# Kernel tuning notes

Hardware: AMD Instinct MI355X
Metric: run time of the kernel (lower is better)

The kernel has to match this reference:

```python
import jax, jax.numpy as jnp
import numpy as np

BN_EPS = 1e-5
NORM_EPS = 1e-12  # F.normalize eps
NUM_HEADS = 8
QUERY_DIM = 256
TOP_K = 16


def _l2norm(x):
    n = jnp.linalg.norm(x, axis=-1, keepdims=True)
    return x / jnp.maximum(n, NORM_EPS)


def setup_inputs() -> dict:
    key = jax.random.key(0)
    ks = jax.random.split(key, 8)
    B, S, D, O, N = 2, 512, 1024, 1024, 16384
    return {
        "hidden_states": jax.random.normal(ks[0], (B, S, D), jnp.float32),
        "Wq": jax.random.normal(ks[1], (D, NUM_HEADS * QUERY_DIM), jnp.float32) * 0.02,
        "bq": jnp.zeros((NUM_HEADS * QUERY_DIM,), jnp.float32),
        "bn_gamma": jnp.ones((QUERY_DIM,), jnp.float32),
        "bn_beta": jnp.zeros((QUERY_DIM,), jnp.float32),
        "sub_keys0": jax.random.normal(ks[2], (128, 128), jnp.float32) * 0.02,
        "sub_keys1": jax.random.normal(ks[3], (128, 128), jnp.float32) * 0.02,
        "expert_down": jax.random.normal(ks[4], (N, D), jnp.float32) * 0.02,
        "expert_up": jax.random.normal(ks[5], (N, O), jnp.float32) * 0.02,
    }


def reference(hidden_states, Wq, bq, bn_gamma, bn_beta, sub_keys0, sub_keys1, expert_down, expert_up):
    B, S, D = hidden_states.shape
    H, QD, K = NUM_HEADS, QUERY_DIM, TOP_K

    # query projection -> [B,S,H,QD]
    q = (hidden_states @ Wq + bq).reshape(B, S, H, QD)

    # BatchNorm1d over flattened (B*S*H, QD), training-mode batch stats (biased var)
    qf = q.reshape(-1, QD)
    mean = qf.mean(axis=0)
    var = qf.var(axis=0)
    qf = (qf - mean) * jax.lax.rsqrt(var + BN_EPS) * bn_gamma + bn_beta
    q = qf.reshape(B, S, H, QD)

    # split query into two halves, L2-normalize queries and keys, sub-scores
    half = QD // 2
    s0 = jnp.einsum('bshd,nd->bshn', _l2norm(q[..., :half]), _l2norm(sub_keys0))  # [B,S,H,128]
    s1 = jnp.einsum('bshd,nd->bshn', _l2norm(q[..., half:]), _l2norm(sub_keys1))  # [B,S,H,128]

    # cartesian-product scores: flat expert idx = i*128 + j (matches meshgrid 'ij')
    total = (s0[..., :, None] + s1[..., None, :]).reshape(B, S, H, -1)  # [B,S,H,16384]

    top_scores, top_idx = jax.lax.top_k(total, K)  # [B,S,H,K]
    w = jax.nn.softmax(top_scores, axis=-1)

    dw = expert_down[top_idx]  # [B,S,H,K,D]  (expert_hidden_size = 1)
    uw = expert_up[top_idx]    # [B,S,H,K,O]

    ei = jnp.einsum('bshkd,bsd->bshk', dw, hidden_states)  # per-expert scalar hidden
    eo = jax.nn.gelu(ei, approximate=False)                # F.gelu default = erf
    out = jnp.einsum('bshko,bshk,bshk->bso', uw, eo, w)    # weighted sum over K and H
    return out
```

## Files before the change

kernel.cpp:

```cpp
#include <hip/hip_runtime.h>
#include <math.h>

typedef unsigned long long u64;
typedef unsigned int u32;
typedef unsigned short ushort_t;
typedef _Float16 half8 __attribute__((ext_vector_type(8)));
typedef float f32x4 __attribute__((ext_vector_type(4)));

#define TOKENS 1024
#define DDIM   1024
#define NHEAD  8
#define QD     256
#define HQD    2048
#define NROWS  8192
#define NKEY   128
#define TOPK   16

#define QSCALE 256.0f
#define QINVS  (1.0f / 65536.0f)

__device__ __forceinline__ ushort_t f2bf(float f) {
    u32 u = __float_as_uint(f);
    u32 r = (u + 0x7FFFu + ((u >> 16) & 1u)) >> 16;
    return (ushort_t)r;
}
__device__ __forceinline__ float bf_lo(u32 w) { return __uint_as_float(w << 16); }
__device__ __forceinline__ float bf_hi(u32 w) { return __uint_as_float(w & 0xFFFF0000u); }

__device__ __forceinline__ void hsplit(float x, ushort_t& h, ushort_t& l) {
    _Float16 hh = (_Float16)x;
    float r = x - (float)hh;
    _Float16 ll = (_Float16)r;
    union { _Float16 f; ushort_t u; } c1, c2;
    c1.f = hh; c2.f = ll;
    h = c1.u; l = c2.u;
}

__device__ __forceinline__ u32 ordf(float v) {
    u32 u = __float_as_uint(v);
    return (u & 0x80000000u) ? ~u : (u | 0x80000000u);
}
__device__ __forceinline__ u64 mkkey2(float v, u32 idx) {
    return ((u64)ordf(v) << 32) | (u64)(0xFFFFFFFFu - idx);
}

template<int NTHR, int ITERS>
__device__ __forceinline__ void cvt_chunk(int gcb, int tid,
                                          const float* __restrict__ down,
                                          const float* __restrict__ up,
                                          ushort_t* __restrict__ downb,
                                          ushort_t* __restrict__ upb) {
    const float* src = (gcb < 1024) ? down : up;
    ushort_t* dst = (gcb < 1024) ? downb : upb;
    const size_t base4 = (size_t)(gcb & 1023) * 4096;
    const float4* s4 = (const float4*)src;
    ushort4* d4 = (ushort4*)dst;
#pragma unroll 4
    for (int it = 0; it < ITERS; it++) {
        size_t i = base4 + (size_t)it * NTHR + tid;
        float4 v = s4[i];
        ushort4 o;
        o.x = f2bf(v.x); o.y = f2bf(v.y); o.z = f2bf(v.z); o.w = f2bf(v.w);
        d4[i] = o;
    }
}

__global__ __launch_bounds__(256) void k_prep1(
    const float* __restrict__ A, const float* __restrict__ W,
    ushort_t* __restrict__ Ab, ushort_t* __restrict__ Wt,
    const float* __restrict__ sk0, const float* __restrict__ sk1,
    float* __restrict__ k0n, float* __restrict__ k1n)
{
    __shared__ __align__(16) char praw[18464];
    const int bid = blockIdx.x;
    const int tid = threadIdx.x;

    if (bid < 128) {
#pragma unroll
        for (int i = 0; i < 8; i++) {
            const int row = bid * 8 + i;
            float4 v = *(const float4*)(A + (size_t)row * 1024 + tid * 4);
            ushort4 h, l;
            hsplit(v.x * QSCALE, h.x, l.x);
            hsplit(v.y * QSCALE, h.y, l.y);
            hsplit(v.z * QSCALE, h.z, l.z);
            hsplit(v.w * QSCALE, h.w, l.w);
            *(ushort4*)(Ab + (size_t)row * 2048 + tid * 4) = h;
            *(ushort4*)(Ab + (size_t)row * 2048 + 1024 + tid * 4) = l;
        }
    } else if (bid < 640) {
        const int cb = bid - 128;
        const int k0 = (cb >> 5) * 64;
        const int n0 = (cb & 31) * 64;
        ushort_t* Lh = (ushort_t*)praw;
        ushort_t* Ll = (ushort_t*)praw + 4608;
        const int nn = (tid & 15) * 4;
        const int kk = tid >> 4;
#pragma unroll
        for (int p = 0; p < 4; p++) {
            const int k = kk + 16 * p;
            float4 v = *(const float4*)(W + (size_t)(k0 + k) * HQD + n0 + nn);
            float xs[4] = {v.x * QSCALE, v.y * QSCALE, v.z * QSCALE, v.w * QSCALE};
#pragma unroll
            for (int j = 0; j < 4; j++) {
                ushort_t h, l;
                hsplit(xs[j], h, l);
                Lh[(nn + j) * 72 + k] = h;
                Ll[(nn + j) * 72 + k] = l;
            }
        }
        __syncthreads();
#pragma unroll
        for (int e = 0; e < 2; e++) {
            const int idx = tid + 256 * e;
            const int n = idx >> 3, ks = idx & 7;
            uint4 hv = *(const uint4*)(Lh + n * 72 + ks * 8);
            uint4 lv = *(const uint4*)(Ll + n * 72 + ks * 8);
            *(uint4*)(Wt + (size_t)(n0 + n) * 2048 + k0 + ks * 8) = hv;
            *(uint4*)(Wt + (size_t)(n0 + n) * 2048 + 1024 + k0 + ks * 8) = lv;
        }
    } else {
        float* fs = (float*)praw;
        const int b2 = bid - 640;
        const int sub = tid >> 7;
        const int col = tid & 127;
        const int gr = b2 * 2 + sub;
        const float* src = (gr < 128) ? sk0 : sk1;
        float* dst = (gr < 128) ? k0n : k1n;
        const int row = gr & 127;
        float v = src[row * 128 + col];
        float sq = v * v;
        for (int off = 32; off; off >>= 1) sq += __shfl_down(sq, off);
        if ((tid & 63) == 0) fs[tid >> 6] = sq;
        __syncthreads();
        if ((tid & 127) == 0) {
            float n = sqrtf(fs[tid >> 6] + fs[(tid >> 6) + 1]);
            fs[8 + sub] = 1.0f / fmaxf(n, 1e-12f);
        }
        __syncthreads();
        dst[row * 128 + col] = v * fs[8 + sub];
    }
}

__global__ __launch_bounds__(256) void k_fused2(
    const ushort_t* __restrict__ Ab, const ushort_t* __restrict__ Wt,
    float* __restrict__ qp,
    const float* __restrict__ down, const float* __restrict__ up,
    ushort_t* __restrict__ downb, ushort_t* __restrict__ upb)
{
    __shared__ __align__(16) char lds[2][16384];
    const int tid = threadIdx.x;
    const int bid = blockIdx.x;

    if (bid >= 512) {
        cvt_chunk<256, 16>(bid - 512, tid, down, up, downb, upb);
        return;
    }

    const int m0 = (bid >> 5) * 64;
    const int n0 = (bid & 31) * 64;

    const int srow = tid >> 2;
    const int scol = (tid & 3) * 16;
    const int swz = (srow & 7) << 4;

    const int lane = tid & 63;
    const int w = tid >> 6;
    const int wmb = (w >> 1) * 32;
    const int wnb = (w & 1) * 32;
    const int fr = lane & 15;
    const int kg = lane >> 4;
    const int rswz = (fr & 7) << 4;

    f32x4 acc[2][2];
#pragma unroll
    for (int i = 0; i < 2; i++)
#pragma unroll
        for (int j = 0; j < 2; j++)
            acc[i][j] = (f32x4){0.f, 0.f, 0.f, 0.f};

    uint4 ar0, ar1, br0, br1;

    auto LOADR = [&](int gs) {
        const int term = gs >> 4;
        const int aoff = (term == 1) ? 1024 : 0;
        const int woff = (term == 2) ? 1024 : 0;
        const int kb = (gs & 15) * 64;
        const ushort_t* ap = Ab + (size_t)(m0 + srow) * 2048 + aoff + kb + scol;
        const ushort_t* wp = Wt + (size_t)(n0 + srow) * 2048 + woff + kb + scol;
        ar0 = *(const uint4*)(ap);
        ar1 = *(const uint4*)(ap + 8);
        br0 = *(const uint4*)(wp);
        br1 = *(const uint4*)(wp + 8);
    };
    auto WLDS = [&](int buf) {
        char* As = lds[buf];
        char* Bs = lds[buf] + 8192;
        const int b0 = (srow * 128 + scol * 2) ^ swz;
        const int b1 = (srow * 128 + scol * 2 + 16) ^ swz;
        *(uint4*)(As + b0) = ar0;
        *(uint4*)(As + b1) = ar1;
        *(uint4*)(Bs + b0) = br0;
        *(uint4*)(Bs + b1) = br1;
    };

    LOADR(0);
    WLDS(0);

    for (int s = 0; s < 48; s++) {
        __syncthreads();
        if (s < 47) LOADR(s + 1);
        const char* As = lds[s & 1];
        const char* Bs = lds[s & 1] + 8192;
#pragma unroll
        for (int kh = 0; kh < 2; kh++) {
            half8 a[2], b[2];
#pragma unroll
            for (int f = 0; f < 2; f++) {
                const int rowA = wmb + f * 16 + fr;
                a[f] = *(const half8*)(As + ((rowA * 128 + kh * 64 + kg * 16) ^ rswz));
                const int rowB = wnb + f * 16 + fr;
                b[f] = *(const half8*)(Bs + ((rowB * 128 + kh * 64 + kg * 16) ^ rswz));
            }
#pragma unroll
            for (int fm = 0; fm < 2; fm++)
#pragma unroll
                for (int fn = 0; fn < 2; fn++)
                    acc[fm][fn] = __builtin_amdgcn_mfma_f32_16x16x32_f16(
                        a[fm], b[fn], acc[fm][fn], 0, 0, 0);
        }
        if (s < 47) WLDS((s + 1) & 1);
    }

#pragma unroll
    for (int fm = 0; fm < 2; fm++) {
        const int rbase = m0 + wmb + fm * 16 + kg * 4;
#pragma unroll
        for (int fn = 0; fn < 2; fn++) {
            const int c = n0 + wnb + fn * 16 + fr;
#pragma unroll
            for (int j = 0; j < 4; j++)
                qp[(size_t)(rbase + j) * HQD + c] = acc[fm][fn][j];
        }
    }
}

__global__ __launch_bounds__(256) void k_bnstat1(const float* __restrict__ qp,
                                                 const float* __restrict__ bq,
                                                 float* __restrict__ psum,
                                                 float* __restrict__ psq,
                                                 float qsc,
                                                 const float* __restrict__ down,
                                                 const float* __restrict__ up,
                                                 ushort_t* __restrict__ downb,
                                                 ushort_t* __restrict__ upb)
{
    const int b = blockIdx.x;
    const int j = threadIdx.x;
    if (b >= 512) {
        cvt_chunk<256, 16>(512 + (b - 512), j, down, up, downb, upb);
        return;
    }
    float s = 0.f, sq = 0.f;
#pragma unroll 4
    for (int rr = 0; rr < 16; rr++) {
        const int r = b * 16 + rr;
        const size_t g = (size_t)r * 256 + j;
        float v = qp[g] * qsc + bq[(r & 7) * 256 + j];
        s += v; sq += v * v;
    }
    psum[b * 256 + j] = s;
    psq[b * 256 + j]  = sq;
}

__global__ __launch_bounds__(256) void k_bnstat2(const float* __restrict__ psum,
                                                 const float* __restrict__ psq,
                                                 const float* __restrict__ gamma,
                                                 float* __restrict__ meanOut,
                                                 float* __restrict__ scaleOut)
{
    __shared__ float ls[8][64];
    const int col = blockIdx.x * 32 + (threadIdx.x & 31);
    const int seg = threadIdx.x >> 5;
    float s = 0.f, sq = 0.f;
    for (int b = seg; b < 512; b += 8) {
        s += psum[b * 256 + col];
        sq += psq[b * 256 + col];
    }
    ls[seg][(threadIdx.x & 31)] = s;
    ls[seg][32 + (threadIdx.x & 31)] = sq;
    __syncthreads();
    if (threadIdx.x < 32) {
        float ts = 0.f, tq = 0.f;
#pragma unroll
        for (int g = 0; g < 8; g++) {
            ts += ls[g][threadIdx.x];
            tq += ls[g][32 + threadIdx.x];
        }
        float mean = ts * (1.0f / 8192.0f);
        float var = tq * (1.0f / 8192.0f) - mean * mean;
        meanOut[col] = mean;
        scaleOut[col] = gamma[col] / sqrtf(var + 1e-5f);
    }
}

__global__ __launch_bounds__(256) void k_scores(const float* __restrict__ qp,
                                                const float* __restrict__ bq,
                                                const float* __restrict__ mean,
                                                const float* __restrict__ scale,
                                                const float* __restrict__ beta,
                                                const float* __restrict__ kn0,
                                                const float* __restrict__ kn1,
                                                float* __restrict__ sOut0,
                                                float* __restrict__ sOut1,
                                                float qsc,
                                                const float* __restrict__ down,
                                                const float* __restrict__ up,
                                                ushort_t* __restrict__ downb,
                                                ushort_t* __restrict__ upb)
{
    __shared__ float Qs[128 * 68];
    __shared__ float Ks[64 * 132];
    __shared__ float rp[4][64];
    __shared__ float invn[64];
    const int bid = blockIdx.x;
    const int tid = threadIdx.x;
    if (bid >= 256) {
        cvt_chunk<256, 16>(768 + (bid - 256), tid, down, up, downb, upb);
        return;
    }
    const int half = bid >> 7;
    const int row0 = (bid & 127) * 64;

    {
        const int d4 = (tid & 31) * 4;
        const int rbase = tid >> 5;
        const int j4 = half * 128 + d4;
        float4 m4 = *(const float4*)(mean + j4);
        float4 sc4 = *(const float4*)(scale + j4);
        float4 be4 = *(const float4*)(beta + j4);
        float4 bi4 = *(const float4*)(bq + rbase * 256 + j4);
#pragma unroll
        for (int p = 0; p < 8; p++) {
            const int rr = rbase + p * 8;
            const int row = row0 + rr;
            const size_t g = (size_t)(row >> 3) * 2048 + (size_t)rbase * 256 + j4;
            float4 a = *(const float4*)(qp + g);
            float x0 = (a.x * qsc + bi4.x - m4.x) * sc4.x + be4.x;
            float x1 = (a.y * qsc + bi4.y - m4.y) * sc4.y + be4.y;
            float x2 = (a.z * qsc + bi4.z - m4.z) * sc4.z + be4.z;
            float x3 = (a.w * qsc + bi4.w - m4.w) * sc4.w + be4.w;
            Qs[(d4 + 0) * 68 + rr] = x0;
            Qs[(d4 + 1) * 68 + rr] = x1;
            Qs[(d4 + 2) * 68 + rr] = x2;
            Qs[(d4 + 3) * 68 + rr] = x3;
        }
    }
    __syncthreads();
    {
        const int r = tid & 63, qd = tid >> 6;
        float s = 0.f;
#pragma unroll 8
        for (int d = qd * 32; d < qd * 32 + 32; d++) {
            float v = Qs[d * 68 + r];
            s += v * v;
        }
        rp[qd][r] = s;
    }
    __syncthreads();
    if (tid < 64) {
        float s = rp[0][tid] + rp[1][tid] + rp[2][tid] + rp[3][tid];
        invn[tid] = 1.0f / fmaxf(sqrtf(s), 1e-12f);
    }

    const float* kn = half ? kn1 : kn0;
    float* sOut = half ? sOut1 : sOut0;
    const int ty = tid >> 5;
    const int tx = tid & 31;
    float acc[8][4] = {};

    for (int c = 0; c < 2; c++) {
        __syncthreads();
        {
            int dd4 = (tid & 15) * 4;
            int n = tid >> 4;
#pragma unroll
            for (int p = 0; p < 8; p++) {
                int nn = n + p * 16;
                float4 v = *(const float4*)(kn + nn * 128 + c * 64 + dd4);
                Ks[(dd4 + 0) * 132 + nn] = v.x; Ks[(dd4 + 1) * 132 + nn] = v.y;
                Ks[(dd4 + 2) * 132 + nn] = v.z; Ks[(dd4 + 3) * 132 + nn] = v.w;
            }
        }
        __syncthreads();
#pragma unroll
        for (int d = 0; d < 64; d++) {
            float a[8], b[4];
            *(float4*)(a)     = *(const float4*)&Qs[(c * 64 + d) * 68 + ty * 8];
            *(float4*)(a + 4) = *(const float4*)&Qs[(c * 64 + d) * 68 + ty * 8 + 4];
            *(float4*)(b)     = *(const float4*)&Ks[d * 132 + tx * 4];
#pragma unroll
            for (int i = 0; i < 8; i++)
#pragma unroll
                for (int j = 0; j < 4; j++)
                    acc[i][j] = fmaf(a[i], b[j], acc[i][j]);
        }
    }
#pragma unroll
    for (int i = 0; i < 8; i++) {
        const float iv = invn[ty * 8 + i];
        float4 r;
        r.x = acc[i][0] * iv; r.y = acc[i][1] * iv;
        r.z = acc[i][2] * iv; r.w = acc[i][3] * iv;
        *(float4*)(sOut + (size_t)(row0 + ty * 8 + i) * 128 + tx * 4) = r;
    }
}

__global__ __launch_bounds__(256) void k_topk(const float* __restrict__ s0,
                                              const float* __restrict__ s1,
                                              int* __restrict__ tIdx,
                                              float* __restrict__ tW,
                                              const float* __restrict__ down,
                                              const float* __restrict__ up,
                                              ushort_t* __restrict__ downb,
                                              ushort_t* __restrict__ upb)
{
    __shared__ float shv[4][2][16];
    __shared__ int   shi[4][2][16];
    __shared__ float swv[4][16];
    __shared__ u32   swi[4][16];
    const int bid = blockIdx.x;
    if (bid >= 2048) {
        cvt_chunk<256, 16>(1536 + (bid - 2048), threadIdx.x, down, up, downb, upb);
        return;
    }
    const int w = threadIdx.x >> 6;
    const int lane = threadIdx.x & 63;
    const int row = bid * 4 + w;
    const u64 below = (1ULL << lane) - 1;

    float v0[2], v1[2];
    u32 o0[2], o1[2], cur[2];
    v0[0] = s0[(size_t)row * 128 + lane];
    v1[0] = s0[(size_t)row * 128 + 64 + lane];
    v0[1] = s1[(size_t)row * 128 + lane];
    v1[1] = s1[(size_t)row * 128 + 64 + lane];
#pragma unroll
    for (int h = 0; h < 2; h++) {
        o0[h] = ordf(v0[h]); o1[h] = ordf(v1[h]); cur[h] = 0u;
    }
    for (int bit = 31; bit >= 0; --bit) {
#pragma unroll
        for (int h = 0; h < 2; h++) {
            u32 cand = cur[h] | (1u << bit);
            int c = __popcll(__ballot(o0[h] >= cand)) + __popcll(__ballot(o1[h] >= cand));
            if (c >= 16) cur[h] = cand;
        }
    }
#pragma unroll
    for (int h = 0; h < 2; h++) {
        u64 g0 = __ballot(o0[h] > cur[h]);
        u64 g1 = __ballot(o1[h] > cur[h]);
        const int cg0 = __popcll(g0);
        const int cntGT = cg0 + __popcll(g1);
        const int need = 16 - cntGT;
        u64 e0 = __ballot(o0[h] == cur[h]);
        u64 e1 = __ballot(o1[h] == cur[h]);
        const int ce0 = __popcll(e0);
        if (o0[h] > cur[h]) {
            int sl = __popcll(g0 & below);
            shv[w][h][sl] = v0[h]; shi[w][h][sl] = lane;
        }
        if (o1[h] > cur[h]) {
            int sl = cg0 + __popcll(g1 & below);
            shv[w][h][sl] = v1[h]; shi[w][h][sl] = lane + 64;
        }
        if (o0[h] == cur[h]) {
            int r = __popcll(e0 & below);
            if (r < need) { shv[w][h][cntGT + r] = v0[h]; shi[w][h][cntGT + r] = lane; }
        }
        if (o1[h] == cur[h]) {
            int r = ce0 + __popcll(e1 & below);
            if (r < need) { shv[w][h][cntGT + r] = v1[h]; shi[w][h][cntGT + r] = lane + 64; }
        }
    }

    float cv[4]; u32 ci[4], co[4];
#pragma unroll
    for (int qq = 0; qq < 4; qq++) {
        int id = lane + 64 * qq;
        int a = id >> 4, b = id & 15;
        cv[qq] = shv[w][0][a] + shv[w][1][b];
        ci[qq] = (u32)(shi[w][0][a] * 128 + shi[w][1][b]);
        co[qq] = ordf(cv[qq]);
    }
    u32 curV = 0;
    for (int bit = 31; bit >= 0; --bit) {
        u32 cand = curV | (1u << bit);
        int c = 0;
#pragma unroll
        for (int qq = 0; qq < 4; qq++) c += __popcll(__ballot(co[qq] >= cand));
        if (c >= 16) curV = cand;
    }
    bool gtf[4], eqf[4];
    int cntGT = 0;
#pragma unroll
    for (int qq = 0; qq < 4; qq++) {
        gtf[qq] = (co[qq] > curV);
        eqf[qq] = (co[qq] == curV);
        cntGT += __popcll(__ballot(gtf[qq]));
    }
    const int need = 16 - cntGT;
    u32 I = 0;
    for (int bit = 13; bit >= 0; --bit) {
        u32 cand = I | ((1u << bit) - 1u);
        int c = 0;
#pragma unroll
        for (int qq = 0; qq < 4; qq++)
            c += __popcll(__ballot(eqf[qq] && (ci[qq] <= cand)));
        if (c < need) I |= (1u << bit);
    }
    int pre = 0;
#pragma unroll
    for (int qq = 0; qq < 4; qq++) {
        bool sel = gtf[qq] || (eqf[qq] && (ci[qq] <= I));
        u64 sm = __ballot(sel);
        if (sel) {
            int sl = pre + __popcll(sm & below);
            swv[w][sl] = cv[qq]; swi[w][sl] = ci[qq];
        }
        pre += __popcll(sm);
    }

    if (lane < 16) {
        float myv = swv[w][lane];
        u32 myi = swi[w][lane];
        u64 myk = mkkey2(myv, myi);
        int rank = 0;
#pragma unroll
        for (int j = 0; j < 16; j++) {
            u64 kj = mkkey2(swv[w][j], swi[w][j]);
            rank += (kj > myk);
        }
        float vmax = myv;
#pragma unroll
        for (int off = 1; off < 16; off <<= 1)
            vmax = fmaxf(vmax, __shfl_xor(vmax, off, 16));
        float e = expf(myv - vmax);
        float ssum = e;
#pragma unroll
        for (int off = 1; off < 16; off <<= 1) ssum += __shfl_xor(ssum, off, 16);
        tW[(size_t)row * 16 + rank] = e / ssum;
        tIdx[(size_t)row * 16 + rank] = (int)myi;
    }
}

__global__ __launch_bounds__(1024) void k_mlp_bf(const float* __restrict__ hidden,
                                                 const ushort_t* __restrict__ downb,
                                                 const ushort_t* __restrict__ upb,
                                                 const int* __restrict__ tIdx,
                                                 const float* __restrict__ tW,
                                                 float* __restrict__ out)
{
    __shared__ float cf[128];
    __shared__ int   ei[128];
    __shared__ float part[3 * 1024];
    const int t = blockIdx.x;
    const int tid = threadIdx.x;
    const int wave = tid >> 6, lane = tid & 63;

    if (tid < 128) ei[tid] = tIdx[(size_t)t * 128 + tid];

    const float* hp = hidden + (size_t)t * 1024;
    float h[16];
    *(float4*)(h + 0)  = *(const float4*)(hp + lane * 8);
    *(float4*)(h + 4)  = *(const float4*)(hp + lane * 8 + 4);
    *(float4*)(h + 8)  = *(const float4*)(hp + 512 + lane * 8);
    *(float4*)(h + 12) = *(const float4*)(hp + 512 + lane * 8 + 4);

#pragma unroll
    for (int g = 0; g < 2; g++) {
        const int pg = wave * 8 + g * 4;
        float s[4];
        uint4 a[4], b[4];
#pragma unroll
        for (int i = 0; i < 4; i++) {
            const int e = tIdx[(size_t)t * 128 + pg + i];
            const uint4* rp = (const uint4*)(downb + (size_t)e * 1024);
            a[i] = rp[lane];
            b[i] = rp[lane + 64];
        }
#pragma unroll
        for (int i = 0; i < 4; i++) {
            float acc = 0.f;
            const u32* aw = (const u32*)&a[i];
            const u32* bw = (const u32*)&b[i];
#pragma unroll
            for (int c = 0; c < 4; c++) {
                acc = fmaf(bf_lo(aw[c]), h[2 * c], acc);
                acc = fmaf(bf_hi(aw[c]), h[2 * c + 1], acc);
                acc = fmaf(bf_lo(bw[c]), h[8 + 2 * c], acc);
                acc = fmaf(bf_hi(bw[c]), h[8 + 2 * c + 1], acc);
            }
            s[i] = acc;
        }
#pragma unroll
        for (int i = 0; i < 4; i++)
#pragma unroll
            for (int off = 1; off < 64; off <<= 1) s[i] += __shfl_xor(s[i], off);
        if (lane < 4) {
            float x = (lane == 0) ? s[0] : (lane == 1) ? s[1] : (lane == 2) ? s[2] : s[3];
            float wv = tW[(size_t)t * 128 + pg + lane];
            float gl = 0.5f * x * (1.0f + erff(x * 0.70710678118654752f));
            cf[pg + lane] = wv * gl;
        }
    }
    __syncthreads();

    const int q = tid >> 8;
    const int jl = (tid & 255) * 4;
    float acc[4] = {};
    const int p0 = q * 32;
#pragma unroll 8
    for (int p = p0; p < p0 + 32; p++) {
        const float c = cf[p];
        uint2 v = *(const uint2*)(upb + (size_t)ei[p] * 1024 + jl);
        acc[0] = fmaf(c, bf_lo(v.x), acc[0]);
        acc[1] = fmaf(c, bf_hi(v.x), acc[1]);
        acc[2] = fmaf(c, bf_lo(v.y), acc[2]);
        acc[3] = fmaf(c, bf_hi(v.y), acc[3]);
    }
    if (q) *(float4*)&part[(q - 1) * 1024 + jl] = *(float4*)acc;
    __syncthreads();
    if (q == 0) {
        float4 p0v = *(float4*)&part[jl];
        float4 p1v = *(float4*)&part[1024 + jl];
        float4 p2v = *(float4*)&part[2048 + jl];
        float4 r;
        r.x = acc[0] + p0v.x + p1v.x + p2v.x;
        r.y = acc[1] + p0v.y + p1v.y + p2v.y;
        r.z = acc[2] + p0v.z + p1v.z + p2v.z;
        r.w = acc[3] + p0v.w + p1v.w + p2v.w;
        *(float4*)(out + (size_t)t * 1024 + jl) = r;
    }
}

__global__ __launch_bounds__(1024) void k_coef_f32(const float* __restrict__ hidden,
                                                   const float* __restrict__ down,
                                                   const int* __restrict__ tIdx,
                                                   const float* __restrict__ tW,
                                                   float* __restrict__ coef)
{
    __shared__ __align__(16) float hs[1024];
    __shared__ int   eidx[128];
    __shared__ float wv[128];
    const int t = blockIdx.x;
    const int tid = threadIdx.x;
    hs[tid] = hidden[(size_t)t * 1024 + tid];
    if (tid < 128) {
        eidx[tid] = tIdx[(size_t)t * 128 + tid];
        wv[tid]   = tW[(size_t)t * 128 + tid];
    }
    __syncthreads();
    const int wave = tid >> 6, lane = tid & 63;
#pragma unroll 2
    for (int i = 0; i < 8; i++) {
        const int p = wave * 8 + i;
        const float4* dp = (const float4*)(down + (size_t)eidx[p] * 1024);
        float sum = 0.f;
#pragma unroll
        for (int c = 0; c < 4; c++) {
            float4 dv = dp[lane + 64 * c];
            float4 hv = *(const float4*)(hs + (lane + 64 * c) * 4);
            sum += dv.x * hv.x + dv.y * hv.y + dv.z * hv.z + dv.w * hv.w;
        }
        for (int off = 32; off; off >>= 1) sum += __shfl_down(sum, off);
        if (lane == 0) {
            float x = sum;
            float g = 0.5f * x * (1.0f + erff(x * 0.70710678118654752f));
            coef[(size_t)t * 128 + p] = wv[p] * g;
        }
    }
}

__global__ __launch_bounds__(256) void k_accum_f32(const float* __restrict__ up,
                                                   const int* __restrict__ tIdx,
                                                   const float* __restrict__ coef,
                                                   float* __restrict__ out)
{
    __shared__ float cf[128];
    __shared__ int   ei[128];
    const int t = blockIdx.x >> 2;
    const int c = blockIdx.x & 3;
    const int tid = threadIdx.x;
    if (tid < 128) {
        cf[tid] = coef[(size_t)t * 128 + tid];
        ei[tid] = tIdx[(size_t)t * 128 + tid];
    }
    __syncthreads();
    const int j = c * 256 + tid;
    float acc = 0.f;
#pragma unroll 8
    for (int p = 0; p < 128; p++)
        acc = fmaf(cf[p], up[(size_t)ei[p] * 1024 + j], acc);
    out[(size_t)t * 1024 + j] = acc;
}

__global__ __launch_bounds__(256) void k_fall1(
    const float* __restrict__ A, const float* __restrict__ W,
    float* __restrict__ qp,
    const float* __restrict__ sk0, const float* __restrict__ sk1,
    float* __restrict__ k0n, float* __restrict__ k1n)
{
    __shared__ float smem[2 * 32 * 68];
    const int bid = blockIdx.x;
    const int tid = threadIdx.x;

    if (bid < 512) {
        float* As = smem;
        float* Bs = smem + 32 * 68;
        const int m0 = (bid >> 5) * 64;
        const int n0 = (bid & 31) * 64;
        const int aM  = tid >> 3;
        const int aK4 = (tid & 7) * 4;
        const int bK  = tid >> 4;
        const int bN4 = (tid & 15) * 4;
        const int ty  = tid >> 4;
        const int tx  = tid & 15;
        float acc[4][4] = {};
        for (int kk = 0; kk < 1024; kk += 32) {
            __syncthreads();
#pragma unroll
            for (int p = 0; p < 2; p++) {
                int m = aM + 32 * p;
                float4 v = *(const float4*)(A + (size_t)(m0 + m) * DDIM + kk + aK4);
                As[(aK4 + 0) * 68 + m] = v.x; As[(aK4 + 1) * 68 + m] = v.y;
                As[(aK4 + 2) * 68 + m] = v.z; As[(aK4 + 3) * 68 + m] = v.w;
            }
#pragma unroll
            for (int p = 0; p < 2; p++) {
                int k = bK + 16 * p;
                float4 v = *(const float4*)(W + (size_t)(kk + k) * HQD + n0 + bN4);
                *(float4*)&Bs[k * 68 + bN4] = v;
            }
            __syncthreads();
#pragma unroll
            for (int k = 0; k < 32; k++) {
                float a[4], b[4];
                *(float4*)(a) = *(const float4*)&As[k * 68 + ty * 4];
                *(float4*)(b) = *(const float4*)&Bs[k * 68 + tx * 4];
#pragma unroll
                for (int i = 0; i < 4; i++)
#pragma unroll
                    for (int j = 0; j < 4; j++)
                        acc[i][j] = fmaf(a[i], b[j], acc[i][j]);
            }
        }
#pragma unroll
        for (int i = 0; i < 4; i++) {
            int m = m0 + ty * 4 + i;
            float4 r;
            r.x = acc[i][0]; r.y = acc[i][1]; r.z = acc[i][2]; r.w = acc[i][3];
            *(float4*)(qp + (size_t)m * HQD + n0 + tx * 4) = r;
        }
    } else {
        const int b2 = bid - 512;
        const int sub = tid >> 7;
        const int col = tid & 127;
        const int gr = b2 * 2 + sub;
        const float* src = (gr < 128) ? sk0 : sk1;
        float* dst = (gr < 128) ? k0n : k1n;
        const int row = gr & 127;
        float v = src[row * 128 + col];
        float sq = v * v;
        for (int off = 32; off; off >>= 1) sq += __shfl_down(sq, off);
        if ((tid & 63) == 0) smem[tid >> 6] = sq;
        __syncthreads();
        if ((tid & 127) == 0) {
            float n = sqrtf(smem[tid >> 6] + smem[(tid >> 6) + 1]);
            smem[8 + sub] = 1.0f / fmaxf(n, 1e-12f);
        }
        __syncthreads();
        dst[row * 128 + col] = v * smem[8 + sub];
    }
}

extern "C" void kernel_launch(void* const* d_in, const int* in_sizes, int n_in,
                              void* d_out, int out_size, void* d_ws, size_t ws_size,
                              hipStream_t stream)
{
    const float* hidden = (const float*)d_in[0];
    const float* Wq     = (const float*)d_in[1];
    const float* bq     = (const float*)d_in[2];
    const float* gamma  = (const float*)d_in[3];
    const float* beta   = (const float*)d_in[4];
    const float* sk0    = (const float*)d_in[5];
    const float* sk1    = (const float*)d_in[6];
    const float* down   = (const float*)d_in[7];
    const float* up     = (const float*)d_in[8];
    float* out = (float*)d_out;

    float* ws = (float*)d_ws;
    size_t o = 0;
    float* qp    = ws + o; o += (size_t)TOKENS * HQD;
    float* ps    = ws + o; o += 512 * 256;
    float* pq    = ws + o; o += 512 * 256;
    float* meanb = ws + o; o += 256;
    float* scaleb= ws + o; o += 256;
    float* k0n   = ws + o; o += NKEY * 128;
    float* k1n   = ws + o; o += NKEY * 128;
    float* s0    = ws + o; o += (size_t)NROWS * 128;
    float* s1    = ws + o; o += (size_t)NROWS * 128;
    float* tW    = ws + o; o += (size_t)NROWS * TOPK;
    int*   tIdx  = (int*)(ws + o); o += (size_t)NROWS * TOPK;
    float* coef  = ws + o; o += (size_t)TOKENS * 128;
    ushort_t* downb = (ushort_t*)(ws + o); o += (size_t)16384 * 1024 / 2;
    ushort_t* upb   = (ushort_t*)(ws + o); o += (size_t)16384 * 1024 / 2;
    ushort_t* Ab    = (ushort_t*)(ws + o); o += (size_t)1024 * 2048 / 2;
    ushort_t* Wt    = (ushort_t*)(ws + o); o += (size_t)2048 * 2048 / 2;
    const int useBF = (ws_size >= o * sizeof(float)) ? 1 : 0;
    const float qsc = useBF ? QINVS : 1.0f;

    if (useBF) {
        k_prep1 <<<768, 256, 0, stream>>>(hidden, Wq, Ab, Wt, sk0, sk1, k0n, k1n);
        k_fused2<<<1024, 256, 0, stream>>>(Ab, Wt, qp, down, up, downb, upb);
        k_bnstat1<<<768, 256, 0, stream>>>(qp, bq, ps, pq, qsc, down, up, downb, upb);
        k_bnstat2<<<8, 256, 0, stream>>>(ps, pq, gamma, meanb, scaleb);
        k_scores <<<1024, 256, 0, stream>>>(qp, bq, meanb, scaleb, beta,
                                            k0n, k1n, s0, s1, qsc,
                                            down, up, downb, upb);
        k_topk   <<<2560, 256, 0, stream>>>(s0, s1, tIdx, tW, down, up, downb, upb);
        k_mlp_bf <<<TOKENS, 1024, 0, stream>>>(hidden, downb, upb, tIdx, tW, out);
    } else {
        k_fall1 <<<640, 256, 0, stream>>>(hidden, Wq, qp, sk0, sk1, k0n, k1n);
        k_bnstat1<<<512, 256, 0, stream>>>(qp, bq, ps, pq, qsc, down, up, downb, upb);
        k_bnstat2<<<8, 256, 0, stream>>>(ps, pq, gamma, meanb, scaleb);
        k_scores <<<256, 256, 0, stream>>>(qp, bq, meanb, scaleb, beta,
                                           k0n, k1n, s0, s1, qsc,
                                           down, up, downb, upb);
        k_topk   <<<2048, 256, 0, stream>>>(s0, s1, tIdx, tW, down, up, downb, upb);
        k_coef_f32 <<<TOKENS, 1024, 0, stream>>>(hidden, down, tIdx, tW, coef);
        k_accum_f32<<<4096, 256, 0, stream>>>(up, tIdx, coef, out);
    }
}
```

Before: 186.8 us.

## Rebalance bf16 expert conversion across kernels and widen up-projection loads

The fp32-to-bf16 conversion chunks for the expert tables are moved out of the BN-stat kernel. More of them now ride along in the GEMM kernel's extra blocks, and the score kernel's chunk range and grid are shifted to match. The up-projection accumulation in the MLP kernel now uses 16-byte loads, 8 outputs per thread and 8 partial groups instead of 4, which needs more shared memory for the reduction. The aim is to hide more conversion work behind the GEMM and get better memory-level parallelism in the gather, at the cost of a larger LDS footprint and register use.

```diff
diff --git a/kernel.cpp b/kernel.cpp
--- a/kernel.cpp
+++ b/kernel.cpp
@@ -249,18 +249,10 @@
                                                  const float* __restrict__ bq,
                                                  float* __restrict__ psum,
                                                  float* __restrict__ psq,
-                                                 float qsc,
-                                                 const float* __restrict__ down,
-                                                 const float* __restrict__ up,
-                                                 ushort_t* __restrict__ downb,
-                                                 ushort_t* __restrict__ upb)
+                                                 float qsc)
 {
     const int b = blockIdx.x;
     const int j = threadIdx.x;
-    if (b >= 512) {
-        cvt_chunk<256, 16>(512 + (b - 512), j, down, up, downb, upb);
-        return;
-    }
     float s = 0.f, sq = 0.f;
 #pragma unroll 4
     for (int rr = 0; rr < 16; rr++) {
@@ -326,7 +318,7 @@
     const int bid = blockIdx.x;
     const int tid = threadIdx.x;
     if (bid >= 256) {
-        cvt_chunk<256, 16>(768 + (bid - 256), tid, down, up, downb, upb);
+        cvt_chunk<256, 16>(1024 + (bid - 256), tid, down, up, downb, upb);
         return;
     }
     const int half = bid >> 7;
@@ -564,7 +556,7 @@
 {
     __shared__ float cf[128];
     __shared__ int   ei[128];
-    __shared__ float part[3 * 1024];
+    __shared__ float part[7 * 1024];
     const int t = blockIdx.x;
     const int tid = threadIdx.x;
     const int wave = tid >> 6, lane = tid & 63;
@@ -617,31 +609,40 @@
     }
     __syncthreads();
 
-    const int q = tid >> 8;
-    const int jl = (tid & 255) * 4;
-    float acc[4] = {};
-    const int p0 = q * 32;
-#pragma unroll 8
-    for (int p = p0; p < p0 + 32; p++) {
+    const int g8 = tid >> 7;
+    const int jl = (tid & 127) * 8;
+    float acc[8] = {};
+    const int p0 = g8 * 16;
+#pragma unroll 4
+    for (int p = p0; p < p0 + 16; p++) {
         const float c = cf[p];
-        uint2 v = *(const uint2*)(upb + (size_t)ei[p] * 1024 + jl);
+        uint4 v = *(const uint4*)(upb + (size_t)ei[p] * 1024 + jl);
         acc[0] = fmaf(c, bf_lo(v.x), acc[0]);
         acc[1] = fmaf(c, bf_hi(v.x), acc[1]);
         acc[2] = fmaf(c, bf_lo(v.y), acc[2]);
         acc[3] = fmaf(c, bf_hi(v.y), acc[3]);
-    }
-    if (q) *(float4*)&part[(q - 1) * 1024 + jl] = *(float4*)acc;
+        acc[4] = fmaf(c, bf_lo(v.z), acc[4]);
+        acc[5] = fmaf(c, bf_hi(v.z), acc[5]);
+        acc[6] = fmaf(c, bf_lo(v.w), acc[6]);
+        acc[7] = fmaf(c, bf_hi(v.w), acc[7]);
+    }
+    if (g8) {
+        *(float4*)&part[(g8 - 1) * 1024 + jl]     = *(float4*)(acc);
+        *(float4*)&part[(g8 - 1) * 1024 + jl + 4] = *(float4*)(acc + 4);
+    }
     __syncthreads();
-    if (q == 0) {
-        float4 p0v = *(float4*)&part[jl];
-        float4 p1v = *(float4*)&part[1024 + jl];
-        float4 p2v = *(float4*)&part[2048 + jl];
-        float4 r;
-        r.x = acc[0] + p0v.x + p1v.x + p2v.x;
-        r.y = acc[1] + p0v.y + p1v.y + p2v.y;
-        r.z = acc[2] + p0v.z + p1v.z + p2v.z;
-        r.w = acc[3] + p0v.w + p1v.w + p2v.w;
-        *(float4*)(out + (size_t)t * 1024 + jl) = r;
+    if (g8 == 0) {
+        float4 r0 = *(float4*)(acc);
+        float4 r1 = *(float4*)(acc + 4);
+#pragma unroll
+        for (int p = 0; p < 7; p++) {
+            float4 a0 = *(float4*)&part[p * 1024 + jl];
+            float4 a1 = *(float4*)&part[p * 1024 + jl + 4];
+            r0.x += a0.x; r0.y += a0.y; r0.z += a0.z; r0.w += a0.w;
+            r1.x += a1.x; r1.y += a1.y; r1.z += a1.z; r1.w += a1.w;
+        }
+        *(float4*)(out + (size_t)t * 1024 + jl)     = r0;
+        *(float4*)(out + (size_t)t * 1024 + jl + 4) = r1;
     }
 }
 
@@ -823,17 +824,17 @@
 
     if (useBF) {
         k_prep1 <<<768, 256, 0, stream>>>(hidden, Wq, Ab, Wt, sk0, sk1, k0n, k1n);
-        k_fused2<<<1024, 256, 0, stream>>>(Ab, Wt, qp, down, up, downb, upb);
-        k_bnstat1<<<768, 256, 0, stream>>>(qp, bq, ps, pq, qsc, down, up, downb, upb);
+        k_fused2<<<1536, 256, 0, stream>>>(Ab, Wt, qp, down, up, downb, upb);
+        k_bnstat1<<<512, 256, 0, stream>>>(qp, bq, ps, pq, qsc);
         k_bnstat2<<<8, 256, 0, stream>>>(ps, pq, gamma, meanb, scaleb);
-        k_scores <<<1024, 256, 0, stream>>>(qp, bq, meanb, scaleb, beta,
-                                            k0n, k1n, s0, s1, qsc,
-                                            down, up, downb, upb);
+        k_scores <<<768, 256, 0, stream>>>(qp, bq, meanb, scaleb, beta,
+                                           k0n, k1n, s0, s1, qsc,
+                                           down, up, downb, upb);
         k_topk   <<<2560, 256, 0, stream>>>(s0, s1, tIdx, tW, down, up, downb, upb);
         k_mlp_bf <<<TOKENS, 1024, 0, stream>>>(hidden, downb, upb, tIdx, tW, out);
     } else {
         k_fall1 <<<640, 256, 0, stream>>>(hidden, Wq, qp, sk0, sk1, k0n, k1n);
-        k_bnstat1<<<512, 256, 0, stream>>>(qp, bq, ps, pq, qsc, down, up, downb, upb);
+        k_bnstat1<<<512, 256, 0, stream>>>(qp, bq, ps, pq, qsc);
         k_bnstat2<<<8, 256, 0, stream>>>(ps, pq, gamma, meanb, scaleb);
         k_scores <<<256, 256, 0, stream>>>(qp, bq, meanb, scaleb, beta,
                                            k0n, k1n, s0, s1, qsc,
```

Result: faster. 183.2 us, median of 2 (-2.0%).
